# Kernel optimization log

Hardware: AMD Instinct MI355X
Metric: run time of the kernel (lower is better)

Reference implementation:

```python
import jax, jax.numpy as jnp
import numpy as np

N_NODES = 262144
N_EDGES = 524288
N_GRAPHS = 8192
BN_EPS = 1e-5


def setup_inputs() -> dict:
    key = jax.random.key(0)
    ks = jax.random.split(key, 12)
    x = jax.random.normal(ks[0], (N_NODES, 77), dtype=jnp.float32)
    edge_index = jax.random.randint(ks[1], (2, N_EDGES), 0, N_NODES, dtype=jnp.int32)
    # sorted segment ids covering every graph (arange-style fill)
    batch = (jnp.arange(N_NODES, dtype=jnp.int32) * N_GRAPHS // N_NODES).astype(jnp.int32)
    s77 = 1.0 / np.sqrt(77.0)
    s128 = 1.0 / np.sqrt(128.0)
    return {
        "x": x,
        "edge_index": edge_index,
        "batch": batch,
        "w0a": jax.random.normal(ks[2], (77, 128), dtype=jnp.float32) * s77,
        "b0a": jnp.zeros((128,), jnp.float32),
        "w0b": jax.random.normal(ks[3], (128, 128), dtype=jnp.float32) * s128,
        "b0b": jnp.zeros((128,), jnp.float32),
        "wa": jax.random.normal(ks[4], (4, 128, 128), dtype=jnp.float32) * s128,
        "ba": jnp.zeros((4, 128), jnp.float32),
        "wb": jax.random.normal(ks[5], (4, 128, 128), dtype=jnp.float32) * s128,
        "bb": jnp.zeros((4, 128), jnp.float32),
        "gamma": jnp.ones((5, 128), jnp.float32),
        "beta": jnp.zeros((5, 128), jnp.float32),
    }


def _gin_encoder(x, edge_index, batch, w0a, b0a, w0b, b0b, wa, ba, wb, bb, gamma, beta):
    n = x.shape[0]
    src, dst = edge_index[0], edge_index[1]
    h = x
    pooled = []
    for i in range(5):
        # GINConv (eps=0): agg_i = h_i + sum_{(j,i) in E} h_j, then 2-layer MLP
        agg = h + jax.ops.segment_sum(h[src], dst, num_segments=n)
        if i == 0:
            w1, c1, w2, c2 = w0a, b0a, w0b, b0b
        else:
            w1, c1, w2, c2 = wa[i - 1], ba[i - 1], wb[i - 1], bb[i - 1]
        h = jax.nn.relu(agg @ w1 + c1) @ w2 + c2
        h = jax.nn.relu(h)
        # BatchNorm1d (training-mode batch statistics, biased variance)
        mean = jnp.mean(h, axis=0)
        var = jnp.mean(jnp.square(h - mean), axis=0)
        h = gamma[i] * (h - mean) * jax.lax.rsqrt(var + BN_EPS) + beta[i]
        pooled.append(jax.ops.segment_max(h, batch, num_segments=N_GRAPHS))
    return jnp.concatenate(pooled, axis=1)  # [N_GRAPHS, 640]


def reference(x, edge_index, batch, w0a, b0a, w0b, b0b, wa, ba, wb, bb, gamma, beta):
    return _gin_encoder(x, edge_index, batch, w0a, b0a, w0b, b0b, wa, ba, wb, bb, gamma, beta)
```

## Files before the change

### kernel.cpp

```cpp
#include <hip/hip_runtime.h>
#include <cstdint>
#include <cstddef>

#define N_NODES_C 262144
#define N_EDGES_C 524288
#define N_GRAPHS_C 8192
#define BN_EPS_C 1e-5f

typedef short short8 __attribute__((ext_vector_type(8)));
typedef float f32x4 __attribute__((ext_vector_type(4)));

union Frag { int2 p2[2]; short8 v8; };

__device__ __forceinline__ unsigned short f2bf(float f) {
  unsigned int u = __float_as_uint(f);
  u += 0x7fffu + ((u >> 16) & 1u);
  return (unsigned short)(u >> 16);
}
__device__ __forceinline__ float bf2f(unsigned short h) {
  return __uint_as_float(((unsigned int)h) << 16);
}

__global__ __launch_bounds__(256) void hist_kernel(const int* __restrict__ dst, int* __restrict__ cnt) {
  int e = blockIdx.x * 256 + threadIdx.x;
  if (e < N_EDGES_C) atomicAdd(&cnt[dst[e]], 1);
}

__global__ __launch_bounds__(256) void scanA_kernel(const int* __restrict__ cnt,
                                                    int* __restrict__ rs, int* __restrict__ bsums) {
  __shared__ int lds[256];
  const int b = blockIdx.x, t = threadIdx.x;
  int4 v = ((const int4*)(cnt + b * 1024))[t];
  lds[t] = v.x + v.y + v.z + v.w;
  __syncthreads();
  for (int off = 1; off < 256; off <<= 1) {
    int add = (t >= off) ? lds[t - off] : 0;
    __syncthreads();
    lds[t] += add;
    __syncthreads();
  }
  int excl = (t > 0) ? lds[t - 1] : 0;
  if (t == 255) bsums[b] = lds[255];
  int4 o;
  o.x = excl; o.y = excl + v.x; o.z = excl + v.x + v.y; o.w = excl + v.x + v.y + v.z;
  ((int4*)(rs + b * 1024))[t] = o;
}

__global__ __launch_bounds__(256) void scanB_kernel(int* __restrict__ bsums) {
  __shared__ int lds[256];
  const int t = threadIdx.x;
  lds[t] = bsums[t];
  __syncthreads();
  for (int off = 1; off < 256; off <<= 1) {
    int add = (t >= off) ? lds[t - off] : 0;
    __syncthreads();
    lds[t] += add;
    __syncthreads();
  }
  bsums[t] = (t > 0) ? lds[t - 1] : 0;
}

__global__ __launch_bounds__(256) void scanC_kernel(int* __restrict__ rs, int* __restrict__ cursor,
                                                    const int* __restrict__ bsums) {
  int i = blockIdx.x * 256 + threadIdx.x;
  int v = rs[i] + bsums[i >> 10];
  rs[i] = v;
  cursor[i] = v;
  if (i == 0) rs[N_NODES_C] = N_EDGES_C;
}

__global__ __launch_bounds__(256) void edge_bucket_kernel(const int* __restrict__ src,
                                                          const int* __restrict__ dst,
                                                          int* __restrict__ cursor,
                                                          int* __restrict__ ebuf) {
  int e = blockIdx.x * 256 + threadIdx.x;
  if (e >= N_EDGES_C) return;
  int pos = atomicAdd(&cursor[dst[e]], 1);
  ebuf[pos] = src[e];
}

__global__ __launch_bounds__(256) void agg77_kernel(const float* __restrict__ x,
                                                    const int* __restrict__ rs,
                                                    const int* __restrict__ ebuf,
                                                    float* __restrict__ agg) {
  int idx = blockIdx.x * 256 + threadIdx.x;
  int n = idx >> 5, q = idx & 31;
  int s = rs[n], e = rs[n + 1];
  const size_t nb = (size_t)n * 77;
  float v0 = x[nb + q];
  float v1 = x[nb + q + 32];
  float v2 = (q < 13) ? x[nb + q + 64] : 0.f;
  for (int i = s; i < e; ++i) {
    const size_t sb = (size_t)ebuf[i] * 77;
    v0 += x[sb + q];
    v1 += x[sb + q + 32];
    if (q < 13) v2 += x[sb + q + 64];
  }
  const size_t ob = (size_t)n * 128;
  agg[ob + q] = v0;
  agg[ob + q + 32] = v1;
  agg[ob + q + 64] = (q < 13) ? v2 : 0.f;
  agg[ob + q + 96] = 0.f;
}

__global__ __launch_bounds__(256) void aggbn_kernel(const float4* __restrict__ h4,
                                                    const int* __restrict__ rs,
                                                    const int* __restrict__ ebuf,
                                                    const float* __restrict__ S,
                                                    const float* __restrict__ gamma,
                                                    const float* __restrict__ beta,
                                                    float4* __restrict__ out4) {
  int idx = blockIdx.x * 256 + threadIdx.x;
  int n = idx >> 5, q = idx & 31;
  const float inv_n = 1.0f / (float)N_NODES_C;
  float sc[4], sh[4];
#pragma unroll
  for (int j = 0; j < 4; ++j) {
    int f = q * 4 + j;
    float mean = S[f] * inv_n;
    float var = S[128 + f] * inv_n - mean * mean;
    float s = gamma[f] * rsqrtf(var + BN_EPS_C);
    sc[j] = s;
    sh[j] = beta[f] - mean * s;
  }
  int s0 = rs[n], e0 = rs[n + 1];
  float4 v = h4[(size_t)n * 32 + q];
  for (int i = s0; i < e0; ++i) {
    float4 u = h4[(size_t)ebuf[i] * 32 + q];
    v.x += u.x; v.y += u.y; v.z += u.z; v.w += u.w;
  }
  float cnt = (float)(e0 - s0 + 1);
  v.x = v.x * sc[0] + cnt * sh[0];
  v.y = v.y * sc[1] + cnt * sh[1];
  v.z = v.z * sc[2] + cnt * sh[2];
  v.w = v.w * sc[3] + cnt * sh[3];
  out4[(size_t)n * 32 + q] = v;
}

__global__ __launch_bounds__(256) void wsplit_kernel(const float* __restrict__ w0a,
                                                     const float* __restrict__ w0b,
                                                     const float* __restrict__ wa,
                                                     const float* __restrict__ wb,
                                                     unsigned short* __restrict__ Wpk) {
  int tid = blockIdx.x * 256 + threadIdx.x;
  int m = tid >> 11;
  int rem = tid & 2047;
  int f = rem >> 6;
  int l = rem & 63;
  int ct = f >> 2, ks = f & 3;
  int c = ct * 16 + (l & 15);
  const size_t mb = (size_t)m * 32768;
  const size_t fl = (size_t)(f * 64 + l) * 4;
#pragma unroll
  for (int j = 0; j < 8; ++j) {
    int k = ks * 32 + ((l >> 4) << 3) + j;
    float w;
    if (m == 0)      w = (k < 77) ? w0a[k * 128 + c] : 0.f;
    else if (m == 1) w = w0b[k * 128 + c];
    else if (m < 6)  w = wa[(size_t)(m - 2) * 16384 + k * 128 + c];
    else             w = wb[(size_t)(m - 6) * 16384 + k * 128 + c];
    unsigned short hh = f2bf(w);
    unsigned short ll = f2bf(w - bf2f(hh));
    if (j < 4) {
      Wpk[mb + fl + j] = hh;
      Wpk[mb + 16384 + fl + j] = ll;
    } else {
      Wpk[mb + 8192 + fl + (j - 4)] = hh;
      Wpk[mb + 24576 + fl + (j - 4)] = ll;
    }
  }
}

__global__ __launch_bounds__(512, 2) void mlp_kernel(float* __restrict__ H,
                                                     const unsigned short* __restrict__ W1pk,
                                                     const unsigned short* __restrict__ W2pk,
                                                     const float* __restrict__ b1,
                                                     const float* __restrict__ b2,
                                                     float* __restrict__ Sout,
                                                     float* __restrict__ gmax,
                                                     float* __restrict__ gmin) {
  __shared__ int4 sW2[4096];
  __shared__ int4 sW1C[4096];
  __shared__ float gmM[8][128];
  __shared__ float gmN[8][128];
  __shared__ float bsum[128];
  __shared__ float bsq[128];

  const int t = threadIdx.x;
  const int lane = t & 63;
  const int wv = t >> 6;
  const int cb = lane & 15;
  const int g = lane >> 4;

  {
    const int4* s2 = (const int4*)W2pk;
#pragma unroll
    for (int i = 0; i < 8; ++i) sW2[t + i * 512] = s2[t + i * 512];
  }

  float bc1[8], bc2[8];
#pragma unroll
  for (int ct = 0; ct < 8; ++ct) {
    bc1[ct] = b1[ct * 16 + cb];
    bc2[ct] = b2[ct * 16 + cb];
  }

  float ssum[8] = {}, ssq[8] = {};
  const size_t blockRow0 = (size_t)blockIdx.x * 1024;

  f32x4 va[8];
  {
    const float* hp = H + (blockRow0 + wv * 16 + cb) * 128 + g * 8;
#pragma unroll
    for (int q = 0; q < 8; ++q)
      va[q] = *(const f32x4*)(hp + (q >> 1) * 32 + (q & 1) * 4);
  }

  for (int it = 0; it < 8; ++it) {
    const size_t strip = blockRow0 + it * 128;
    const size_t wrow0 = strip + wv * 16;

    __syncthreads();
    {
      const int4* s1 = (const int4*)W1pk;
#pragma unroll
      for (int i = 0; i < 8; ++i) sW1C[t + i * 512] = s1[t + i * 512];
    }

    Frag ah[4], al[4];
#pragma unroll
    for (int ks = 0; ks < 4; ++ks) {
#pragma unroll
      for (int j = 0; j < 8; ++j) {
        float fv = va[ks * 2 + (j >> 2)][j & 3];
        unsigned short hh = f2bf(fv);
        ah[ks].v8[j] = (short)hh;
        al[ks].v8[j] = (short)f2bf(fv - bf2f(hh));
      }
    }

    __syncthreads();

    f32x4 d1[8] = {};
    {
      const int2* R1 = (const int2*)sW1C;
#pragma unroll
      for (int ks = 0; ks < 4; ++ks) {
#pragma unroll
        for (int ct = 0; ct < 8; ++ct) {
          int fi = (ct * 4 + ks) * 64 + lane;
          Frag wh, wl;
          wh.p2[0] = R1[fi];        wh.p2[1] = R1[2048 + fi];
          wl.p2[0] = R1[4096 + fi]; wl.p2[1] = R1[6144 + fi];
          d1[ct] = __builtin_amdgcn_mfma_f32_16x16x32_bf16(ah[ks].v8, wh.v8, d1[ct], 0, 0, 0);
          d1[ct] = __builtin_amdgcn_mfma_f32_16x16x32_bf16(al[ks].v8, wh.v8, d1[ct], 0, 0, 0);
          d1[ct] = __builtin_amdgcn_mfma_f32_16x16x32_bf16(ah[ks].v8, wl.v8, d1[ct], 0, 0, 0);
        }
      }
    }
    __syncthreads();

    if (it < 7) {
      const float* hp = H + (blockRow0 + (it + 1) * 128 + wv * 16 + cb) * 128 + g * 8;
#pragma unroll
      for (int q = 0; q < 8; ++q)
        va[q] = *(const f32x4*)(hp + (q >> 1) * 32 + (q & 1) * 4);
    }

    {
      char* c1b = (char*)sW1C;
#pragma unroll
      for (int ct = 0; ct < 8; ++ct) {
#pragma unroll
        for (int j = 0; j < 4; ++j) {
          int r = wv * 16 + g * 4 + j;
          int c = ct * 16 + cb;
          float v = fmaxf(d1[ct][j] + bc1[ct], 0.f);
          *(float*)(c1b + ((r * 512 + c * 4) ^ ((r & 7) << 4))) = v;
        }
      }
    }
    __syncthreads();

    f32x4 d2[8] = {};
    {
      const int rr = wv * 16 + cb;
      const char* c1r = (const char*)sW1C;
      const int2* R2 = (const int2*)sW2;
#pragma unroll
      for (int ks = 0; ks < 4; ++ks) {
        int base = rr * 512 + ks * 128 + g * 32;
        f32x4 x0 = *(const f32x4*)(c1r + ((base) ^ ((rr & 7) << 4)));
        f32x4 x1 = *(const f32x4*)(c1r + ((base + 16) ^ ((rr & 7) << 4)));
        Frag a2h, a2l;
#pragma unroll
        for (int j = 0; j < 8; ++j) {
          float fv = (j < 4) ? x0[j] : x1[j - 4];
          unsigned short hh = f2bf(fv);
          a2h.v8[j] = (short)hh;
          a2l.v8[j] = (short)f2bf(fv - bf2f(hh));
        }
#pragma unroll
        for (int ct = 0; ct < 8; ++ct) {
          int fi = (ct * 4 + ks) * 64 + lane;
          Frag wh, wl;
          wh.p2[0] = R2[fi];        wh.p2[1] = R2[2048 + fi];
          wl.p2[0] = R2[4096 + fi]; wl.p2[1] = R2[6144 + fi];
          d2[ct] = __builtin_amdgcn_mfma_f32_16x16x32_bf16(a2h.v8, wh.v8, d2[ct], 0, 0, 0);
          d2[ct] = __builtin_amdgcn_mfma_f32_16x16x32_bf16(a2l.v8, wh.v8, d2[ct], 0, 0, 0);
          d2[ct] = __builtin_amdgcn_mfma_f32_16x16x32_bf16(a2h.v8, wl.v8, d2[ct], 0, 0, 0);
        }
      }
    }

#pragma unroll
    for (int ct = 0; ct < 8; ++ct) {
      const int c = ct * 16 + cb;
      float mx = 0.f;
      float mn = 3.4e38f;
#pragma unroll
      for (int j = 0; j < 4; ++j) {
        size_t r = wrow0 + g * 4 + j;
        float v = fmaxf(d2[ct][j] + bc2[ct], 0.f);
        H[r * 128 + c] = v;
        ssum[ct] += v;
        ssq[ct] += v * v;
        mx = fmaxf(mx, v);
        mn = fminf(mn, v);
      }
      mx = fmaxf(mx, __shfl_xor(mx, 16));
      mx = fmaxf(mx, __shfl_xor(mx, 32));
      mn = fminf(mn, __shfl_xor(mn, 16));
      mn = fminf(mn, __shfl_xor(mn, 32));
      if (lane < 16) { gmM[wv][c] = mx; gmN[wv][c] = mn; }
    }
    __syncthreads();

    {
      int gl = t >> 7, f = t & 127;
      size_t gg = (strip >> 5) + gl;
      gmax[gg * 128 + f] = fmaxf(gmM[2 * gl][f], gmM[2 * gl + 1][f]);
      gmin[gg * 128 + f] = fminf(gmN[2 * gl][f], gmN[2 * gl + 1][f]);
    }
  }

  if (t < 128) { bsum[t] = 0.f; bsq[t] = 0.f; }
  __syncthreads();
#pragma unroll
  for (int ct = 0; ct < 8; ++ct) {
    atomicAdd(&bsum[ct * 16 + cb], ssum[ct]);
    atomicAdd(&bsq[ct * 16 + cb], ssq[ct]);
  }
  __syncthreads();
  if (t < 128) {
    atomicAdd(&Sout[t], bsum[t]);
    atomicAdd(&Sout[128 + t], bsq[t]);
  }
}

__global__ __launch_bounds__(256) void pool_kernel(const float* __restrict__ gmax,
                                                   const float* __restrict__ gmin,
                                                   const float* __restrict__ stats,
                                                   const float* __restrict__ gamma,
                                                   const float* __restrict__ beta,
                                                   float* __restrict__ out, int layer) {
  int id = blockIdx.x * 256 + threadIdx.x;
  int gg = id >> 7, f = id & 127;
  const float inv_n = 1.0f / (float)N_NODES_C;
  float mean = stats[f] * inv_n;
  float var = stats[128 + f] * inv_n - mean * mean;
  float sc = gamma[f] * rsqrtf(var + BN_EPS_C);
  float sh = beta[f] - mean * sc;
  float v = (sc >= 0.f ? gmax[id] : gmin[id]) * sc + sh;
  out[(size_t)gg * 640 + layer * 128 + f] = v;
}

extern "C" void kernel_launch(void* const* d_in, const int* in_sizes, int n_in,
                              void* d_out, int out_size, void* d_ws, size_t ws_size,
                              hipStream_t stream) {
  const float* x = (const float*)d_in[0];
  const int* ei = (const int*)d_in[1];
  const int* src = ei;
  const int* dst = ei + N_EDGES_C;
  const float* w0a = (const float*)d_in[3];
  const float* b0a = (const float*)d_in[4];
  const float* w0b = (const float*)d_in[5];
  const float* b0b = (const float*)d_in[6];
  const float* wa = (const float*)d_in[7];
  const float* ba = (const float*)d_in[8];
  const float* wb = (const float*)d_in[9];
  const float* bb = (const float*)d_in[10];
  const float* gamma = (const float*)d_in[11];
  const float* beta = (const float*)d_in[12];
  float* out = (float*)d_out;

  const size_t NNf = (size_t)N_NODES_C * 128;
  float* ws = (float*)d_ws;
  float* Hb0 = ws;
  float* Hb1 = ws + NNf;
  float* STATS = ws + 2 * NNf;
  float* gmax = STATS + 5 * 256;
  float* gmin = gmax + (size_t)N_GRAPHS_C * 128;
  int* cnt = (int*)(gmin + (size_t)N_GRAPHS_C * 128);
  int* rowstart = cnt + N_NODES_C;
  int* cursor = rowstart + N_NODES_C + 4;
  int* bsums = cursor + N_NODES_C;
  int* ebuf = bsums + 256;
  unsigned short* Wpk = (unsigned short*)(((uintptr_t)(ebuf + N_EDGES_C) + 63) & ~(uintptr_t)63);

  wsplit_kernel<<<80, 256, 0, stream>>>(w0a, w0b, wa, wb, Wpk);
  hipMemsetAsync(cnt, 0, N_NODES_C * sizeof(int), stream);
  hipMemsetAsync(STATS, 0, 5 * 256 * sizeof(float), stream);
  hist_kernel<<<N_EDGES_C / 256, 256, 0, stream>>>(dst, cnt);
  scanA_kernel<<<256, 256, 0, stream>>>(cnt, rowstart, bsums);
  scanB_kernel<<<1, 256, 0, stream>>>(bsums);
  scanC_kernel<<<N_NODES_C / 256, 256, 0, stream>>>(rowstart, cursor, bsums);
  edge_bucket_kernel<<<N_EDGES_C / 256, 256, 0, stream>>>(src, dst, cursor, ebuf);

  const int PB = (N_GRAPHS_C * 128) / 256;

  agg77_kernel<<<(N_NODES_C * 32) / 256, 256, 0, stream>>>(x, rowstart, ebuf, Hb1);
  mlp_kernel<<<256, 512, 0, stream>>>(Hb1, Wpk, Wpk + 32768, b0a, b0b,
                                      STATS, gmax, gmin);
  pool_kernel<<<PB, 256, 0, stream>>>(gmax, gmin, STATS, gamma, beta, out, 0);

  float* cur = Hb1;
  float* oth = Hb0;
  for (int i = 1; i < 5; ++i) {
    aggbn_kernel<<<(N_NODES_C * 32) / 256, 256, 0, stream>>>(
        (const float4*)cur, rowstart, ebuf,
        STATS + (size_t)(i - 1) * 256, gamma + (size_t)(i - 1) * 128, beta + (size_t)(i - 1) * 128,
        (float4*)oth);
    mlp_kernel<<<256, 512, 0, stream>>>(oth,
                                        Wpk + (size_t)(1 + i) * 32768,
                                        Wpk + (size_t)(5 + i) * 32768,
                                        ba + (size_t)(i - 1) * 128, bb + (size_t)(i - 1) * 128,
                                        STATS + (size_t)i * 256, gmax, gmin);
    pool_kernel<<<PB, 256, 0, stream>>>(gmax, gmin, STATS + (size_t)i * 256,
                                        gamma + (size_t)i * 128, beta + (size_t)i * 128, out, i);
    float* tmp = cur; cur = oth; oth = tmp;
  }
}
```

Before: 1.931 ms.

## Split fused two-layer MLP kernel into separate GEMM launches with higher occupancy

Replaces the fused MLP kernel, which kept the hidden activation in LDS, with a templated single-GEMM kernel launched twice per layer. The first launch writes the hidden activation in place to global memory and the second computes the output plus BN stats and per-graph max/min. Halving LDS use allows more blocks per CU, and the f32-to-bf16 split now uses the library conversion. The cost is an extra global write and read of the full 262144x128 activation per layer, plus an extra launch.

```diff
diff --git a/kernel.cpp b/kernel.cpp
--- a/kernel.cpp
+++ b/kernel.cpp
@@ -1,4 +1,5 @@
 #include <hip/hip_runtime.h>
+#include <hip/hip_bf16.h>
 #include <cstdint>
 #include <cstddef>
 
@@ -19,6 +20,12 @@
 }
 __device__ __forceinline__ float bf2f(unsigned short h) {
   return __uint_as_float(((unsigned int)h) << 16);
+}
+__device__ __forceinline__ unsigned short f2bf_hw(float f) {
+  __hip_bfloat16 b = __float2bfloat16(f);
+  unsigned short u;
+  __builtin_memcpy(&u, &b, 2);
+  return u;
 }
 
 __global__ __launch_bounds__(256) void hist_kernel(const int* __restrict__ dst, int* __restrict__ cnt) {
@@ -171,16 +178,15 @@
   }
 }
 
-__global__ __launch_bounds__(512, 2) void mlp_kernel(float* __restrict__ H,
-                                                     const unsigned short* __restrict__ W1pk,
-                                                     const unsigned short* __restrict__ W2pk,
-                                                     const float* __restrict__ b1,
-                                                     const float* __restrict__ b2,
-                                                     float* __restrict__ Sout,
-                                                     float* __restrict__ gmax,
-                                                     float* __restrict__ gmin) {
-  __shared__ int4 sW2[4096];
-  __shared__ int4 sW1C[4096];
+template <bool STATS>
+__global__ __launch_bounds__(512, 4) void gemm_kernel(const float* A,
+                                                      float* C,
+                                                      const unsigned short* __restrict__ Wpk,
+                                                      const float* __restrict__ bias,
+                                                      float* __restrict__ Sout,
+                                                      float* __restrict__ gmax,
+                                                      float* __restrict__ gmin) {
+  __shared__ int4 sW[4096];
   __shared__ float gmM[8][128];
   __shared__ float gmN[8][128];
   __shared__ float bsum[128];
@@ -193,150 +199,85 @@
   const int g = lane >> 4;
 
   {
-    const int4* s2 = (const int4*)W2pk;
-#pragma unroll
-    for (int i = 0; i < 8; ++i) sW2[t + i * 512] = s2[t + i * 512];
-  }
-
-  float bc1[8], bc2[8];
-#pragma unroll
-  for (int ct = 0; ct < 8; ++ct) {
-    bc1[ct] = b1[ct * 16 + cb];
-    bc2[ct] = b2[ct * 16 + cb];
-  }
+    const int4* s = (const int4*)Wpk;
+#pragma unroll
+    for (int i = 0; i < 8; ++i) sW[t + i * 512] = s[t + i * 512];
+  }
+  __syncthreads();
+
+  float bc[8];
+#pragma unroll
+  for (int ct = 0; ct < 8; ++ct) bc[ct] = bias[ct * 16 + cb];
 
   float ssum[8] = {}, ssq[8] = {};
   const size_t blockRow0 = (size_t)blockIdx.x * 1024;
-
-  f32x4 va[8];
-  {
-    const float* hp = H + (blockRow0 + wv * 16 + cb) * 128 + g * 8;
-#pragma unroll
-    for (int q = 0; q < 8; ++q)
-      va[q] = *(const f32x4*)(hp + (q >> 1) * 32 + (q & 1) * 4);
-  }
+  const int2* R = (const int2*)sW;
 
   for (int it = 0; it < 8; ++it) {
     const size_t strip = blockRow0 + it * 128;
     const size_t wrow0 = strip + wv * 16;
 
-    __syncthreads();
+    if (STATS && it > 0) __syncthreads();
+
+    Frag ah[4], al[4];
     {
-      const int4* s1 = (const int4*)W1pk;
-#pragma unroll
-      for (int i = 0; i < 8; ++i) sW1C[t + i * 512] = s1[t + i * 512];
-    }
-
-    Frag ah[4], al[4];
-#pragma unroll
-    for (int ks = 0; ks < 4; ++ks) {
-#pragma unroll
-      for (int j = 0; j < 8; ++j) {
-        float fv = va[ks * 2 + (j >> 2)][j & 3];
-        unsigned short hh = f2bf(fv);
-        ah[ks].v8[j] = (short)hh;
-        al[ks].v8[j] = (short)f2bf(fv - bf2f(hh));
-      }
-    }
-
-    __syncthreads();
-
-    f32x4 d1[8] = {};
-    {
-      const int2* R1 = (const int2*)sW1C;
+      const float* hp = A + (wrow0 + cb) * 128 + g * 8;
 #pragma unroll
       for (int ks = 0; ks < 4; ++ks) {
-#pragma unroll
-        for (int ct = 0; ct < 8; ++ct) {
-          int fi = (ct * 4 + ks) * 64 + lane;
-          Frag wh, wl;
-          wh.p2[0] = R1[fi];        wh.p2[1] = R1[2048 + fi];
-          wl.p2[0] = R1[4096 + fi]; wl.p2[1] = R1[6144 + fi];
-          d1[ct] = __builtin_amdgcn_mfma_f32_16x16x32_bf16(ah[ks].v8, wh.v8, d1[ct], 0, 0, 0);
-          d1[ct] = __builtin_amdgcn_mfma_f32_16x16x32_bf16(al[ks].v8, wh.v8, d1[ct], 0, 0, 0);
-          d1[ct] = __builtin_amdgcn_mfma_f32_16x16x32_bf16(ah[ks].v8, wl.v8, d1[ct], 0, 0, 0);
+        f32x4 a0 = *(const f32x4*)(hp + ks * 32);
+        f32x4 a1 = *(const f32x4*)(hp + ks * 32 + 4);
+#pragma unroll
+        for (int j = 0; j < 8; ++j) {
+          float fv = (j < 4) ? a0[j] : a1[j - 4];
+          unsigned short hh = f2bf_hw(fv);
+          ah[ks].v8[j] = (short)hh;
+          al[ks].v8[j] = (short)f2bf_hw(fv - bf2f(hh));
         }
       }
     }
-    __syncthreads();
-
-    if (it < 7) {
-      const float* hp = H + (blockRow0 + (it + 1) * 128 + wv * 16 + cb) * 128 + g * 8;
-#pragma unroll
-      for (int q = 0; q < 8; ++q)
-        va[q] = *(const f32x4*)(hp + (q >> 1) * 32 + (q & 1) * 4);
-    }
-
-    {
-      char* c1b = (char*)sW1C;
+
+    f32x4 acc[8] = {};
+#pragma unroll
+    for (int ks = 0; ks < 4; ++ks) {
 #pragma unroll
       for (int ct = 0; ct < 8; ++ct) {
-#pragma unroll
-        for (int j = 0; j < 4; ++j) {
-          int r = wv * 16 + g * 4 + j;
-          int c = ct * 16 + cb;
-          float v = fmaxf(d1[ct][j] + bc1[ct], 0.f);
-          *(float*)(c1b + ((r * 512 + c * 4) ^ ((r & 7) << 4))) = v;
+        int fi = (ct * 4 + ks) * 64 + lane;
+        Frag wh, wl;
+        wh.p2[0] = R[fi];        wh.p2[1] = R[2048 + fi];
+        wl.p2[0] = R[4096 + fi]; wl.p2[1] = R[6144 + fi];
+        acc[ct] = __builtin_amdgcn_mfma_f32_16x16x32_bf16(ah[ks].v8, wh.v8, acc[ct], 0, 0, 0);
+        acc[ct] = __builtin_amdgcn_mfma_f32_16x16x32_bf16(al[ks].v8, wh.v8, acc[ct], 0, 0, 0);
+        acc[ct] = __builtin_amdgcn_mfma_f32_16x16x32_bf16(ah[ks].v8, wl.v8, acc[ct], 0, 0, 0);
+      }
+    }
+
+#pragma unroll
+    for (int ct = 0; ct < 8; ++ct) {
+      const int c = ct * 16 + cb;
+      float mx = 0.f, mn = 3.4e38f;
+#pragma unroll
+      for (int j = 0; j < 4; ++j) {
+        size_t r = wrow0 + g * 4 + j;
+        float v = fmaxf(acc[ct][j] + bc[ct], 0.f);
+        C[r * 128 + c] = v;
+        if (STATS) {
+          ssum[ct] += v;
+          ssq[ct] += v * v;
+          mx = fmaxf(mx, v);
+          mn = fminf(mn, v);
         }
       }
-    }
-    __syncthreads();
-
-    f32x4 d2[8] = {};
-    {
-      const int rr = wv * 16 + cb;
-      const char* c1r = (const char*)sW1C;
-      const int2* R2 = (const int2*)sW2;
-#pragma unroll
-      for (int ks = 0; ks < 4; ++ks) {
-        int base = rr * 512 + ks * 128 + g * 32;
-        f32x4 x0 = *(const f32x4*)(c1r + ((base) ^ ((rr & 7) << 4)));
-        f32x4 x1 = *(const f32x4*)(c1r + ((base + 16) ^ ((rr & 7) << 4)));
-        Frag a2h, a2l;
-#pragma unroll
-        for (int j = 0; j < 8; ++j) {
-          float fv = (j < 4) ? x0[j] : x1[j - 4];
-          unsigned short hh = f2bf(fv);
-          a2h.v8[j] = (short)hh;
-          a2l.v8[j] = (short)f2bf(fv - bf2f(hh));
-        }
-#pragma unroll
-        for (int ct = 0; ct < 8; ++ct) {
-          int fi = (ct * 4 + ks) * 64 + lane;
-          Frag wh, wl;
-          wh.p2[0] = R2[fi];        wh.p2[1] = R2[2048 + fi];
-          wl.p2[0] = R2[4096 + fi]; wl.p2[1] = R2[6144 + fi];
-          d2[ct] = __builtin_amdgcn_mfma_f32_16x16x32_bf16(a2h.v8, wh.v8, d2[ct], 0, 0, 0);
-          d2[ct] = __builtin_amdgcn_mfma_f32_16x16x32_bf16(a2l.v8, wh.v8, d2[ct], 0, 0, 0);
-          d2[ct] = __builtin_amdgcn_mfma_f32_16x16x32_bf16(a2h.v8, wl.v8, d2[ct], 0, 0, 0);
-        }
+      if (STATS) {
+        mx = fmaxf(mx, __shfl_xor(mx, 16));
+        mx = fmaxf(mx, __shfl_xor(mx, 32));
+        mn = fminf(mn, __shfl_xor(mn, 16));
+        mn = fminf(mn, __shfl_xor(mn, 32));
+        if (lane < 16) { gmM[wv][c] = mx; gmN[wv][c] = mn; }
       }
     }
 
-#pragma unroll
-    for (int ct = 0; ct < 8; ++ct) {
-      const int c = ct * 16 + cb;
-      float mx = 0.f;
-      float mn = 3.4e38f;
-#pragma unroll
-      for (int j = 0; j < 4; ++j) {
-        size_t r = wrow0 + g * 4 + j;
-        float v = fmaxf(d2[ct][j] + bc2[ct], 0.f);
-        H[r * 128 + c] = v;
-        ssum[ct] += v;
-        ssq[ct] += v * v;
-        mx = fmaxf(mx, v);
-        mn = fminf(mn, v);
-      }
-      mx = fmaxf(mx, __shfl_xor(mx, 16));
-      mx = fmaxf(mx, __shfl_xor(mx, 32));
-      mn = fminf(mn, __shfl_xor(mn, 16));
-      mn = fminf(mn, __shfl_xor(mn, 32));
-      if (lane < 16) { gmM[wv][c] = mx; gmN[wv][c] = mn; }
-    }
-    __syncthreads();
-
-    {
+    if (STATS) {
+      __syncthreads();
       int gl = t >> 7, f = t & 127;
       size_t gg = (strip >> 5) + gl;
       gmax[gg * 128 + f] = fmaxf(gmM[2 * gl][f], gmM[2 * gl + 1][f]);
@@ -344,17 +285,19 @@
     }
   }
 
-  if (t < 128) { bsum[t] = 0.f; bsq[t] = 0.f; }
-  __syncthreads();
-#pragma unroll
-  for (int ct = 0; ct < 8; ++ct) {
-    atomicAdd(&bsum[ct * 16 + cb], ssum[ct]);
-    atomicAdd(&bsq[ct * 16 + cb], ssq[ct]);
-  }
-  __syncthreads();
-  if (t < 128) {
-    atomicAdd(&Sout[t], bsum[t]);
-    atomicAdd(&Sout[128 + t], bsq[t]);
+  if (STATS) {
+    if (t < 128) { bsum[t] = 0.f; bsq[t] = 0.f; }
+    __syncthreads();
+#pragma unroll
+    for (int ct = 0; ct < 8; ++ct) {
+      atomicAdd(&bsum[ct * 16 + cb], ssum[ct]);
+      atomicAdd(&bsq[ct * 16 + cb], ssq[ct]);
+    }
+    __syncthreads();
+    if (t < 128) {
+      atomicAdd(&Sout[t], bsum[t]);
+      atomicAdd(&Sout[128 + t], bsq[t]);
+    }
   }
 }
 
@@ -396,8 +339,8 @@
 
   const size_t NNf = (size_t)N_NODES_C * 128;
   float* ws = (float*)d_ws;
-  float* Hb0 = ws;
-  float* Hb1 = ws + NNf;
+  float* RAW = ws;
+  float* WS = ws + NNf;
   float* STATS = ws + 2 * NNf;
   float* gmax = STATS + 5 * 256;
   float* gmin = gmax + (size_t)N_GRAPHS_C * 128;
@@ -417,27 +360,26 @@
   scanC_kernel<<<N_NODES_C / 256, 256, 0, stream>>>(rowstart, cursor, bsums);
   edge_bucket_kernel<<<N_EDGES_C / 256, 256, 0, stream>>>(src, dst, cursor, ebuf);
 
+  const int GB = N_NODES_C / 1024;
   const int PB = (N_GRAPHS_C * 128) / 256;
 
-  agg77_kernel<<<(N_NODES_C * 32) / 256, 256, 0, stream>>>(x, rowstart, ebuf, Hb1);
-  mlp_kernel<<<256, 512, 0, stream>>>(Hb1, Wpk, Wpk + 32768, b0a, b0b,
-                                      STATS, gmax, gmin);
+  agg77_kernel<<<(N_NODES_C * 32) / 256, 256, 0, stream>>>(x, rowstart, ebuf, WS);
+  gemm_kernel<false><<<GB, 512, 0, stream>>>(WS, WS, Wpk, b0a, nullptr, nullptr, nullptr);
+  gemm_kernel<true><<<GB, 512, 0, stream>>>(WS, RAW, Wpk + 32768, b0b, STATS, gmax, gmin);
   pool_kernel<<<PB, 256, 0, stream>>>(gmax, gmin, STATS, gamma, beta, out, 0);
 
-  float* cur = Hb1;
-  float* oth = Hb0;
   for (int i = 1; i < 5; ++i) {
     aggbn_kernel<<<(N_NODES_C * 32) / 256, 256, 0, stream>>>(
-        (const float4*)cur, rowstart, ebuf,
+        (const float4*)RAW, rowstart, ebuf,
         STATS + (size_t)(i - 1) * 256, gamma + (size_t)(i - 1) * 128, beta + (size_t)(i - 1) * 128,
-        (float4*)oth);
-    mlp_kernel<<<256, 512, 0, stream>>>(oth,
-                                        Wpk + (size_t)(1 + i) * 32768,
-                                        Wpk + (size_t)(5 + i) * 32768,
-                                        ba + (size_t)(i - 1) * 128, bb + (size_t)(i - 1) * 128,
-                                        STATS + (size_t)i * 256, gmax, gmin);
+        (float4*)WS);
+    gemm_kernel<false><<<GB, 512, 0, stream>>>(WS, WS, Wpk + (size_t)(1 + i) * 32768,
+                                               ba + (size_t)(i - 1) * 128,
+                                               nullptr, nullptr, nullptr);
+    gemm_kernel<true><<<GB, 512, 0, stream>>>(WS, RAW, Wpk + (size_t)(5 + i) * 32768,
+                                              bb + (size_t)(i - 1) * 128,
+                                              STATS + (size_t)i * 256, gmax, gmin);
     pool_kernel<<<PB, 256, 0, stream>>>(gmax, gmin, STATS + (size_t)i * 256,
                                         gamma + (size_t)i * 128, beta + (size_t)i * 128, out, i);
-    float* tmp = cur; cur = oth; oth = tmp;
-  }
-}
+  }
+}
```

Result: slower. 3.224 ms (+66.9%).
